# Optimization experiments

Hardware: AMD Instinct MI355X
Metric: run time of the kernel (lower is better)

## Reference

```python
import jax, jax.numpy as jnp
import numpy as np

DIM = 512

def setup_inputs() -> dict:
    key = jax.random.key(0)
    ks = jax.random.split(key, 7)
    S = 8192
    scale = 1.0 / np.sqrt(DIM)
    x = jax.random.normal(ks[0], (S, DIM), dtype=jnp.float32)
    # torch.nn.Linear params: weight [out, in], bias [out]
    Wq = jax.random.uniform(ks[1], (DIM, DIM), jnp.float32, -scale, scale)
    bq = jax.random.uniform(ks[2], (DIM,), jnp.float32, -scale, scale)
    Wk = jax.random.uniform(ks[3], (DIM, DIM), jnp.float32, -scale, scale)
    bk = jax.random.uniform(ks[4], (DIM,), jnp.float32, -scale, scale)
    Wv = jax.random.uniform(ks[5], (DIM, DIM), jnp.float32, -scale, scale)
    bv = jax.random.uniform(ks[6], (DIM,), jnp.float32, -scale, scale)
    return {"x": x, "Wq": Wq, "bq": bq, "Wk": Wk, "bk": bk, "Wv": Wv, "bv": bv}

def reference(x, Wq, bq, Wk, bk, Wv, bv):
    S = x.shape[0]
    q = x @ Wq.T + bq  # [S, D]
    k = x @ Wk.T + bk
    v = x @ Wv.T + bv
    scores = (q @ k.T) / jnp.sqrt(jnp.asarray(DIM, x.dtype))  # [S, S]
    causal = jnp.tril(jnp.ones((S, S), dtype=bool))  # keep lower triangle incl. diag
    scores = jnp.where(causal, scores, -jnp.inf)
    attn_weights = jax.nn.softmax(scores, axis=-1)
    output = attn_weights @ v  # [S, D]
    return (output, attn_weights)
```

## Files before the change

kernel.cpp:

```cpp
#include <hip/hip_runtime.h>
#include <hip/hip_bf16.h>
#include <stdint.h>

#define S 8192
#define D 512
#define SCALE 0.044194173824159216f
#define CH 32

typedef __attribute__((ext_vector_type(8))) short short8;
typedef __attribute__((ext_vector_type(4))) float f32x4;

__device__ inline unsigned short f32_to_bf16(float f) {
    union { float f; uint32_t u; } v; v.f = f;
    uint32_t u = v.u;
    return (unsigned short)((u + 0x7FFFu + ((u >> 16) & 1u)) >> 16);
}
__device__ inline float bf2f(unsigned short u) {
    union { float f; uint32_t v; } x; x.v = (uint32_t)u << 16; return x.f;
}
__device__ inline uint2 pack4(float4 v) {
    uint2 p;
    p.x = (uint32_t)f32_to_bf16(v.x) | ((uint32_t)f32_to_bf16(v.y) << 16);
    p.y = (uint32_t)f32_to_bf16(v.z) | ((uint32_t)f32_to_bf16(v.w) << 16);
    return p;
}

__device__ inline void gload16(const void* g, void* l) {
    __builtin_amdgcn_global_load_lds(
        (const __attribute__((address_space(1))) unsigned int*)g,
        (__attribute__((address_space(3))) unsigned int*)l, 16, 0, 0);
}

__device__ inline void stage128x64(const short* __restrict__ src, int ld,
                                   short* dst, int w, int lane) {
#pragma unroll
    for (int j = 0; j < 4; j++) {
        int c = (w * 4 + j) * 64 + lane;
        int row = c >> 3, q = c & 7;
        gload16(src + (size_t)row * ld + q * 8, dst + (size_t)(w * 4 + j) * 512);
    }
}

__device__ inline void mfma_step64(const short* As, const short* Bs,
                                   f32x4 acc[4][4], int wr, int wc, int lane) {
    int rl = lane & 15, kg = lane >> 4;
#pragma unroll
    for (int kk0 = 0; kk0 < 64; kk0 += 32) {
        short8 a[4], b[4];
#pragma unroll
        for (int m = 0; m < 4; m++)
            a[m] = *reinterpret_cast<const short8*>(&As[(wr * 64 + m * 16 + rl) * 64 + kk0 + kg * 8]);
#pragma unroll
        for (int n = 0; n < 4; n++)
            b[n] = *reinterpret_cast<const short8*>(&Bs[(wc * 64 + n * 16 + rl) * 64 + kk0 + kg * 8]);
#pragma unroll
        for (int m = 0; m < 4; m++)
#pragma unroll
            for (int n = 0; n < 4; n++)
                acc[m][n] = __builtin_amdgcn_mfma_f32_16x16x32_bf16(a[m], b[n], acc[m][n], 0, 0, 0);
    }
}

__global__ __launch_bounds__(256) void k_convert(
    const float* __restrict__ x, const float* __restrict__ Wq,
    const float* __restrict__ Wk, const float* __restrict__ Wv,
    short* __restrict__ xb, short* __restrict__ Wb) {
    size_t i4 = (size_t)blockIdx.x * 256 + threadIdx.x;
    const size_t XN4 = (size_t)S * D / 4;
    if (i4 < XN4) {
        float4 v = reinterpret_cast<const float4*>(x)[i4];
        reinterpret_cast<uint2*>(xb)[i4] = pack4(v);
    } else {
        size_t j4 = i4 - XN4;
        size_t w = j4 >> 16;
        size_t rem = j4 & 65535;
        const float* src = (w == 0) ? Wq : ((w == 1) ? Wk : Wv);
        float4 v = reinterpret_cast<const float4*>(src)[rem];
        reinterpret_cast<uint2*>(Wb)[j4] = pack4(v);
    }
}

__global__ __launch_bounds__(256) void k_qkv(
    const short* __restrict__ xb, const short* __restrict__ Wb,
    const float* __restrict__ bq, const float* __restrict__ bk,
    const float* __restrict__ bv, short* __restrict__ QKV) {
    __shared__ __align__(16) short smem[128 * 128];
    short* As = smem;
    short* Bs = smem + 128 * 64;
    int which = blockIdx.z;
    const short* W = Wb + (size_t)which * D * D;
    const float* bias = (which == 0) ? bq : ((which == 1) ? bk : bv);
    short* out = QKV + (size_t)which * S * D;
    int r0 = blockIdx.x * 128, c0 = blockIdx.y * 128;
    int t = threadIdx.x, lane = t & 63, w = t >> 6, wr = w >> 1, wc = w & 1;
    f32x4 acc[4][4];
#pragma unroll
    for (int m = 0; m < 4; m++)
#pragma unroll
        for (int n = 0; n < 4; n++)
#pragma unroll
            for (int j = 0; j < 4; j++) acc[m][n][j] = 0.0f;

    for (int kk = 0; kk < D; kk += 64) {
        __syncthreads();
        stage128x64(xb + (size_t)r0 * D + kk, D, As, w, lane);
        stage128x64(W + (size_t)c0 * D + kk, D, Bs, w, lane);
        __syncthreads();
        mfma_step64(As, Bs, acc, wr, wc, lane);
    }
    __syncthreads();
    short* Es = smem;
    int rg = lane >> 4, cl = lane & 15;
#pragma unroll
    for (int m = 0; m < 4; m++)
#pragma unroll
        for (int n = 0; n < 4; n++) {
            int cloc = wc * 64 + n * 16 + cl;
            float b = bias[c0 + cloc];
#pragma unroll
            for (int jj = 0; jj < 4; jj++) {
                int rloc = wr * 64 + m * 16 + rg * 4 + jj;
                Es[rloc * 128 + cloc] = (short)f32_to_bf16(acc[m][n][jj] + b);
            }
        }
    __syncthreads();
#pragma unroll
    for (int j = 0; j < 8; j++) {
        int c = t + j * 256;
        int row = c >> 4, q = c & 15;
        *reinterpret_cast<uint4*>(&out[(size_t)(r0 + row) * D + c0 + q * 8]) =
            *reinterpret_cast<const uint4*>(&Es[row * 128 + q * 8]);
    }
}

__global__ __launch_bounds__(256) void k_transpose(const short* __restrict__ V,
                                                   short* __restrict__ Vt) {
    __shared__ short tile[64][65];
    int r0 = blockIdx.x * 64;
    int c0 = blockIdx.y * 64;
    int t = threadIdx.x;
#pragma unroll
    for (int j = 0; j < 16; j++) {
        int idx = t + j * 256;
        int r = idx >> 6, c = idx & 63;
        tile[r][c] = V[(size_t)(r0 + r) * D + c0 + c];
    }
    __syncthreads();
#pragma unroll
    for (int j = 0; j < 16; j++) {
        int idx = t + j * 256;
        int rr = idx >> 6, cc = idx & 63;
        Vt[(size_t)(c0 + rr) * S + r0 + cc] = tile[cc][rr];
    }
}

__global__ __launch_bounds__(256) void k_scores(const short* __restrict__ Qb,
                                                const short* __restrict__ Kb,
                                                short* __restrict__ E,
                                                float* __restrict__ pl) {
    int bid = blockIdx.x;
    int bi = 0, bj = 0;
    { int c = 0;
      for (int p = 0; p < 64; p++) { int n = p + 1;
          if (bid < c + n) { bi = p; bj = bid - c; break; } c += n; } }
    int r0 = bi * 128, c0 = bj * 128;
    __shared__ __align__(16) short smem[128 * 128];
    short* As = smem;
    short* Bs = smem + 128 * 64;
    __shared__ float wsum[2][128];
    int t = threadIdx.x, lane = t & 63, w = t >> 6, wr = w >> 1, wc = w & 1;
    f32x4 acc[4][4];
#pragma unroll
    for (int m = 0; m < 4; m++)
#pragma unroll
        for (int n = 0; n < 4; n++)
#pragma unroll
            for (int j = 0; j < 4; j++) acc[m][n][j] = 0.0f;

    for (int kk = 0; kk < D; kk += 64) {
        __syncthreads();
        stage128x64(Qb + (size_t)r0 * D + kk, D, As, w, lane);
        stage128x64(Kb + (size_t)c0 * D + kk, D, Bs, w, lane);
        __syncthreads();
        mfma_step64(As, Bs, acc, wr, wc, lane);
    }
    int rg = lane >> 4, cl = lane & 15;
    bool diag = (bi == bj);
#pragma unroll
    for (int m = 0; m < 4; m++)
#pragma unroll
        for (int jj = 0; jj < 4; jj++) {
            int rloc = wr * 64 + m * 16 + rg * 4 + jj;
            float s4 = 0.f;
#pragma unroll
            for (int n = 0; n < 4; n++) {
                int cloc = wc * 64 + n * 16 + cl;
                float sv = acc[m][n][jj] * SCALE;
                float e = (diag && cloc > rloc) ? 0.0f : __expf(sv);
                acc[m][n][jj] = e;
                s4 += e;
            }
#pragma unroll
            for (int o = 1; o < 16; o <<= 1) s4 += __shfl_xor(s4, o, 64);
            if (cl == 0) wsum[wc][rloc] = s4;
        }
    __syncthreads();
    if (t < 128) pl[(size_t)bj * S + r0 + t] = wsum[0][t] + wsum[1][t];
    short* Es = smem;
#pragma unroll
    for (int m = 0; m < 4; m++)
#pragma unroll
        for (int n = 0; n < 4; n++) {
            int cloc = wc * 64 + n * 16 + cl;
#pragma unroll
            for (int jj = 0; jj < 4; jj++) {
                int rloc = wr * 64 + m * 16 + rg * 4 + jj;
                Es[rloc * 128 + cloc] = (short)f32_to_bf16(acc[m][n][jj]);
            }
        }
    __syncthreads();
#pragma unroll
    for (int j = 0; j < 8; j++) {
        int c = t + j * 256;
        int row = c >> 4, q = c & 15;
        *reinterpret_cast<uint4*>(&E[(size_t)(r0 + row) * S + c0 + q * 8]) =
            *reinterpret_cast<const uint4*>(&Es[row * 128 + q * 8]);
    }
}

__global__ __launch_bounds__(256) void k_combine(const float* __restrict__ pl,
                                                 float* __restrict__ Li) {
    int row = blockIdx.x * 256 + threadIdx.x;
    int nt = (row >> 7) + 1;
    float l = 0.f;
    for (int j = 0; j < nt; j++) l += pl[(size_t)j * S + row];
    Li[row] = 1.0f / l;
}

__global__ __launch_bounds__(256) void k_zero(float* __restrict__ attn) {
    int bid = blockIdx.x;
    int bi = 0, bj = 0;
    { int c = 0;
      for (int p = 0; p < 63; p++) { int n = 63 - p;
          if (bid < c + n) { bi = p; bj = p + 1 + (bid - c); break; } c += n; } }
    int t = threadIdx.x;
    float4 z = make_float4(0.f, 0.f, 0.f, 0.f);
#pragma unroll
    for (int j = 0; j < 16; j++) {
        int c = t + j * 256;
        int row = c >> 5, q = (c & 31) * 4;
        *reinterpret_cast<float4*>(&attn[(size_t)(bi * 128 + row) * S + bj * 128 + q]) = z;
    }
}

__global__ __launch_bounds__(512) void k_pv(const short* __restrict__ E,
                                            const short* __restrict__ Vt,
                                            const float* __restrict__ Li,
                                            float* __restrict__ attn,
                                            float* __restrict__ out) {
    int bid = blockIdx.x;
    int bn = bid & 1, bidx = bid >> 1;
    int panel = 63, chunk = 0;
    { int c = 0;
      for (int p = 63; p >= 0; p--) {
          int nb = (p + 8) >> 3;
          if (bidx < c + nb) { panel = p; chunk = bidx - c; break; } c += nb; } }
    int nst = 4 * (panel + 1);
    int st0 = chunk * CH, st1 = min(nst, st0 + CH);
    int r0 = panel * 128, c0 = bn * 256;
    __shared__ __align__(16) short As[128 * 32];
    __shared__ __align__(16) short Bs[256 * 32];
    __shared__ float Lil[128];
    int t = threadIdx.x;
    if (t < 128) Lil[t] = Li[r0 + t];
    int lane = t & 63, w = t >> 6, wr = w >> 2, wc = w & 3;
    f32x4 acc[4][4];
#pragma unroll
    for (int m = 0; m < 4; m++)
#pragma unroll
        for (int n = 0; n < 4; n++)
#pragma unroll
            for (int j = 0; j < 4; j++) acc[m][n][j] = 0.0f;

    int arow = t >> 2, aq = t & 3;
    bool wrHalf = (bn == 0) ? (arow < 64) : (arow >= 64);

    for (int st = st0; st < st1; ++st) {
        int kk = st * 32;
        __syncthreads();
        { int c = w * 64 + lane; int row = c >> 2, q = c & 3;
          gload16(E + (size_t)(r0 + row) * S + kk + q * 8, As + w * 512); }
#pragma unroll
        for (int j = 0; j < 2; j++) {
            int c = (w * 2 + j) * 64 + lane; int row = c >> 2, q = c & 3;
            gload16(Vt + (size_t)(c0 + row) * S + kk + q * 8, Bs + (size_t)(w * 2 + j) * 512);
        }
        if (wrHalf) {
            const uint4 ev = *reinterpret_cast<const uint4*>(&E[(size_t)(r0 + arow) * S + kk + aq * 8]);
            float li = Lil[arow];
            const unsigned short* es = reinterpret_cast<const unsigned short*>(&ev);
            float4 o0, o1;
            o0.x = bf2f(es[0]) * li; o0.y = bf2f(es[1]) * li;
            o0.z = bf2f(es[2]) * li; o0.w = bf2f(es[3]) * li;
            o1.x = bf2f(es[4]) * li; o1.y = bf2f(es[5]) * li;
            o1.z = bf2f(es[6]) * li; o1.w = bf2f(es[7]) * li;
            float* ap = &attn[(size_t)(r0 + arow) * S + kk + aq * 8];
            *reinterpret_cast<float4*>(ap) = o0;
            *reinterpret_cast<float4*>(ap + 4) = o1;
        }
        __syncthreads();
        int rl = lane & 15, kg = lane >> 4;
        short8 a[4], b[4];
#pragma unroll
        for (int m = 0; m < 4; m++)
            a[m] = *reinterpret_cast<const short8*>(&As[(wr * 64 + m * 16 + rl) * 32 + kg * 8]);
#pragma unroll
        for (int n = 0; n < 4; n++)
            b[n] = *reinterpret_cast<const short8*>(&Bs[(wc * 64 + n * 16 + rl) * 32 + kg * 8]);
#pragma unroll
        for (int m = 0; m < 4; m++)
#pragma unroll
            for (int n = 0; n < 4; n++)
                acc[m][n] = __builtin_amdgcn_mfma_f32_16x16x32_bf16(a[m], b[n], acc[m][n], 0, 0, 0);
    }
    int rg = lane >> 4, cl = lane & 15;
#pragma unroll
    for (int m = 0; m < 4; m++)
#pragma unroll
        for (int n = 0; n < 4; n++) {
            int col = c0 + wc * 64 + n * 16 + cl;
#pragma unroll
            for (int jj = 0; jj < 4; jj++) {
                int rloc = wr * 64 + m * 16 + rg * 4 + jj;
                atomicAdd(&out[(size_t)(r0 + rloc) * D + col], acc[m][n][jj] * Lil[rloc]);
            }
        }
}

extern "C" void kernel_launch(void* const* d_in, const int* in_sizes, int n_in,
                              void* d_out, int out_size, void* d_ws, size_t ws_size,
                              hipStream_t stream) {
    const float* x  = (const float*)d_in[0];
    const float* Wq = (const float*)d_in[1];
    const float* bq = (const float*)d_in[2];
    const float* Wk = (const float*)d_in[3];
    const float* bk = (const float*)d_in[4];
    const float* Wv = (const float*)d_in[5];
    const float* bv = (const float*)d_in[6];
    float* out  = (float*)d_out;
    float* attn = out + (size_t)S * D;

    short* xb  = (short*)d_ws;
    short* Wb  = xb + (size_t)S * D;
    short* QKV = Wb + (size_t)3 * D * D;
    short* Vt  = QKV + (size_t)3 * S * D;
    short* E   = Vt + (size_t)S * D;
    float* pl  = (float*)(E + (size_t)S * S);
    float* Li  = pl + (size_t)64 * S;

    const short* Qb = QKV;
    const short* Kb = QKV + (size_t)S * D;
    const short* Vb = QKV + (size_t)2 * S * D;

    {
        size_t total4 = (size_t)S * D / 4 + (size_t)3 * D * D / 4;
        k_convert<<<dim3((unsigned)(total4 / 256)), 256, 0, stream>>>(x, Wq, Wk, Wv, xb, Wb);
    }
    k_qkv<<<dim3(S / 128, D / 128, 3), 256, 0, stream>>>(xb, Wb, bq, bk, bv, QKV);
    k_transpose<<<dim3(S / 64, D / 64), 256, 0, stream>>>(Vb, Vt);
    k_scores<<<dim3(64 * 65 / 2), 256, 0, stream>>>(Qb, Kb, E, pl);
    k_combine<<<dim3(S / 256), 256, 0, stream>>>(pl, Li);
    k_zero<<<dim3(63 * 64 / 2), 256, 0, stream>>>(attn);
    hipMemsetAsync(d_out, 0, (size_t)S * D * sizeof(float), stream);
    k_pv<<<dim3(2 * 288), 512, 0, stream>>>(E, Vt, Li, attn, out);
}
```

Baseline: 573.9 us.

## Split attention-weight writes out of PV kernel and retile PV GEMM

The normalized attention-weight writes move out of the PV GEMM into a separate k_attn kernel, which also zeroes the upper triangle, so the PV loop only does MMA work. The PV kernel is retiled from 128x256 outputs with 512 threads to 128x128 outputs with 256 threads. It now steps K by 64 through the shared helpers stage128x64/mfma_step64, with 16 steps per chunk. This gives more blocks and cleaner overlap, but E is read once more from global memory and there is an extra kernel launch.

Result: no change. 564.2 us (-1.7%).

```diff
diff --git a/kernel.cpp b/kernel.cpp
--- a/kernel.cpp
+++ b/kernel.cpp
@@ -5,7 +5,7 @@
 #define S 8192
 #define D 512
 #define SCALE 0.044194173824159216f
-#define CH 32
+#define PVCH 16
 
 typedef __attribute__((ext_vector_type(8))) short short8;
 typedef __attribute__((ext_vector_type(4))) float f32x4;
@@ -237,43 +237,65 @@
     Li[row] = 1.0f / l;
 }
 
-__global__ __launch_bounds__(256) void k_zero(float* __restrict__ attn) {
-    int bid = blockIdx.x;
-    int bi = 0, bj = 0;
-    { int c = 0;
-      for (int p = 0; p < 63; p++) { int n = 63 - p;
-          if (bid < c + n) { bi = p; bj = p + 1 + (bid - c); break; } c += n; } }
+__global__ __launch_bounds__(256) void k_attn(const short* __restrict__ E,
+                                              const float* __restrict__ Li,
+                                              float* __restrict__ attn) {
+    int bj = blockIdx.x, bi = blockIdx.y;
+    int r0 = bi * 128, c0 = bj * 128;
     int t = threadIdx.x;
-    float4 z = make_float4(0.f, 0.f, 0.f, 0.f);
-#pragma unroll
-    for (int j = 0; j < 16; j++) {
+    if (bj > bi) {
+        float4 z = make_float4(0.f, 0.f, 0.f, 0.f);
+#pragma unroll
+        for (int j = 0; j < 16; j++) {
+            int c = t + j * 256;
+            int row = c >> 5, q = (c & 31) * 4;
+            *reinterpret_cast<float4*>(&attn[(size_t)(r0 + row) * S + c0 + q]) = z;
+        }
+        return;
+    }
+    __shared__ float Lil[128];
+    if (t < 128) Lil[t] = Li[r0 + t];
+    __syncthreads();
+#pragma unroll
+    for (int j = 0; j < 8; j++) {
         int c = t + j * 256;
-        int row = c >> 5, q = (c & 31) * 4;
-        *reinterpret_cast<float4*>(&attn[(size_t)(bi * 128 + row) * S + bj * 128 + q]) = z;
-    }
-}
-
-__global__ __launch_bounds__(512) void k_pv(const short* __restrict__ E,
+        int row = c >> 4, q = c & 15;
+        uint4 ev = *reinterpret_cast<const uint4*>(&E[(size_t)(r0 + row) * S + c0 + q * 8]);
+        float li = Lil[row];
+        const unsigned short* es = reinterpret_cast<const unsigned short*>(&ev);
+        float4 o0, o1;
+        o0.x = bf2f(es[0]) * li; o0.y = bf2f(es[1]) * li;
+        o0.z = bf2f(es[2]) * li; o0.w = bf2f(es[3]) * li;
+        o1.x = bf2f(es[4]) * li; o1.y = bf2f(es[5]) * li;
+        o1.z = bf2f(es[6]) * li; o1.w = bf2f(es[7]) * li;
+        float* ap = &attn[(size_t)(r0 + row) * S + c0 + q * 8];
+        *reinterpret_cast<float4*>(ap) = o0;
+        *reinterpret_cast<float4*>(ap + 4) = o1;
+    }
+}
+
+__global__ __launch_bounds__(256) void k_pv(const short* __restrict__ E,
                                             const short* __restrict__ Vt,
                                             const float* __restrict__ Li,
-                                            float* __restrict__ attn,
                                             float* __restrict__ out) {
     int bid = blockIdx.x;
-    int bn = bid & 1, bidx = bid >> 1;
+    int bn = bid & 3;
+    int bidx = bid >> 2;
     int panel = 63, chunk = 0;
     { int c = 0;
       for (int p = 63; p >= 0; p--) {
           int nb = (p + 8) >> 3;
           if (bidx < c + nb) { panel = p; chunk = bidx - c; break; } c += nb; } }
-    int nst = 4 * (panel + 1);
-    int st0 = chunk * CH, st1 = min(nst, st0 + CH);
-    int r0 = panel * 128, c0 = bn * 256;
-    __shared__ __align__(16) short As[128 * 32];
-    __shared__ __align__(16) short Bs[256 * 32];
+    int nst = 2 * (panel + 1);
+    int st0 = chunk * PVCH, st1 = min(nst, st0 + PVCH);
+    int r0 = panel * 128, c0 = bn * 128;
+    __shared__ __align__(16) short smem[128 * 128];
+    short* As = smem;
+    short* Bs = smem + 128 * 64;
     __shared__ float Lil[128];
     int t = threadIdx.x;
     if (t < 128) Lil[t] = Li[r0 + t];
-    int lane = t & 63, w = t >> 6, wr = w >> 2, wc = w & 3;
+    int lane = t & 63, w = t >> 6, wr = w >> 1, wc = w & 1;
     f32x4 acc[4][4];
 #pragma unroll
     for (int m = 0; m < 4; m++)
@@ -282,46 +304,13 @@
 #pragma unroll
             for (int j = 0; j < 4; j++) acc[m][n][j] = 0.0f;
 
-    int arow = t >> 2, aq = t & 3;
-    bool wrHalf = (bn == 0) ? (arow < 64) : (arow >= 64);
-
     for (int st = st0; st < st1; ++st) {
-        int kk = st * 32;
-        __syncthreads();
-        { int c = w * 64 + lane; int row = c >> 2, q = c & 3;
-          gload16(E + (size_t)(r0 + row) * S + kk + q * 8, As + w * 512); }
-#pragma unroll
-        for (int j = 0; j < 2; j++) {
-            int c = (w * 2 + j) * 64 + lane; int row = c >> 2, q = c & 3;
-            gload16(Vt + (size_t)(c0 + row) * S + kk + q * 8, Bs + (size_t)(w * 2 + j) * 512);
-        }
-        if (wrHalf) {
-            const uint4 ev = *reinterpret_cast<const uint4*>(&E[(size_t)(r0 + arow) * S + kk + aq * 8]);
-            float li = Lil[arow];
-            const unsigned short* es = reinterpret_cast<const unsigned short*>(&ev);
-            float4 o0, o1;
-            o0.x = bf2f(es[0]) * li; o0.y = bf2f(es[1]) * li;
-            o0.z = bf2f(es[2]) * li; o0.w = bf2f(es[3]) * li;
-            o1.x = bf2f(es[4]) * li; o1.y = bf2f(es[5]) * li;
-            o1.z = bf2f(es[6]) * li; o1.w = bf2f(es[7]) * li;
-            float* ap = &attn[(size_t)(r0 + arow) * S + kk + aq * 8];
-            *reinterpret_cast<float4*>(ap) = o0;
-            *reinterpret_cast<float4*>(ap + 4) = o1;
-        }
-        __syncthreads();
-        int rl = lane & 15, kg = lane >> 4;
-        short8 a[4], b[4];
-#pragma unroll
-        for (int m = 0; m < 4; m++)
-            a[m] = *reinterpret_cast<const short8*>(&As[(wr * 64 + m * 16 + rl) * 32 + kg * 8]);
-#pragma unroll
-        for (int n = 0; n < 4; n++)
-            b[n] = *reinterpret_cast<const short8*>(&Bs[(wc * 64 + n * 16 + rl) * 32 + kg * 8]);
-#pragma unroll
-        for (int m = 0; m < 4; m++)
-#pragma unroll
-            for (int n = 0; n < 4; n++)
-                acc[m][n] = __builtin_amdgcn_mfma_f32_16x16x32_bf16(a[m], b[n], acc[m][n], 0, 0, 0);
+        int kk = st * 64;
+        __syncthreads();
+        stage128x64(E + (size_t)r0 * S + kk, S, As, w, lane);
+        stage128x64(Vt + (size_t)c0 * S + kk, S, Bs, w, lane);
+        __syncthreads();
+        mfma_step64(As, Bs, acc, wr, wc, lane);
     }
     int rg = lane >> 4, cl = lane & 15;
 #pragma unroll
@@ -370,7 +359,7 @@
     k_transpose<<<dim3(S / 64, D / 64), 256, 0, stream>>>(Vb, Vt);
     k_scores<<<dim3(64 * 65 / 2), 256, 0, stream>>>(Qb, Kb, E, pl);
     k_combine<<<dim3(S / 256), 256, 0, stream>>>(pl, Li);
-    k_zero<<<dim3(63 * 64 / 2), 256, 0, stream>>>(attn);
+    k_attn<<<dim3(64, 64), 256, 0, stream>>>(E, Li, attn);
     hipMemsetAsync(d_out, 0, (size_t)S * D * sizeof(float), stream);
-    k_pv<<<dim3(2 * 288), 512, 0, stream>>>(E, Vt, Li, attn, out);
-}
+    k_pv<<<dim3(288 * 4), 256, 0, stream>>>(E, Vt, Li, out);
+}
```
